# Performance work log

Measured on AMD Instinct MI355X. Metric: run time of the kernel, lower is better.

Reference implementation:

```python
import jax, jax.numpy as jnp
import numpy as np

N_NODES = 30000
N_REL = 8
N_EDGES = 150000
EMB = 128
HID = 128
OUT = 256
HEADS = 4
RANK = 8
SCALE = 1.0
NEG_SLOPE = 0.2
LN_EPS = 1e-5


def setup_inputs():
    key = jax.random.key(0)
    ks = jax.random.split(key, 16)
    def nrm(k, shp, s=0.05):
        return jax.random.normal(k, shp, dtype=jnp.float32) * s
    d2 = HEADS * HID  # conv2 input dim = 512
    return {
        "entity_emb": nrm(ks[0], (N_NODES, EMB)),
        "A1": nrm(ks[1], (N_REL, EMB * RANK)),
        "B1": nrm(ks[2], (N_REL, EMB * RANK)),
        "W1": nrm(ks[3], (HEADS * HID, EMB)),
        "att_l1": nrm(ks[4], (1, HEADS, HID)),
        "att_r1": nrm(ks[5], (1, HEADS, HID)),
        "relb1": jnp.zeros((N_REL, HEADS), jnp.float32),
        "bias1": jnp.zeros((HEADS * HID,), jnp.float32),
        "A2": nrm(ks[6], (N_REL, d2 * RANK)),
        "B2": nrm(ks[7], (N_REL, d2 * RANK)),
        "W2": nrm(ks[8], (OUT, d2)),
        "att_l2": nrm(ks[9], (1, 1, OUT)),
        "att_r2": nrm(ks[10], (1, 1, OUT)),
        "relb2": jnp.zeros((N_REL, 1), jnp.float32),
        "bias2": jnp.zeros((OUT,), jnp.float32),
        "res_W": nrm(ks[11], (OUT, EMB)),
        "res_b": jnp.zeros((OUT,), jnp.float32),
        "ln_g": jnp.ones((OUT,), jnp.float32),
        "ln_b": jnp.zeros((OUT,), jnp.float32),
        "edge_index": jax.random.randint(ks[12], (2, N_EDGES), 0, N_NODES),
        "edge_type": jax.random.randint(ks[13], (N_EDGES,), 0, N_REL),
    }


def _rel_gat_conv(x, A, B, W, att_l, att_r, relb, bias, j_idx, i_idx, etype, heads, out_dim, concat):
    # x: [N,d]; A,B: [R, d*k]; W: [heads*out_dim, d]
    N, d = x.shape
    R = A.shape[0]
    k = RANK
    HC = heads * out_dim
    A3 = A.reshape(R, d, k)
    B3 = B.reshape(R, d, k)
    z_all = x @ W.T  # [N, HC] base linear (shared by z_i and z_j)
    # LoRA low-rank projection per (node, relation): P[n,r] = B_r^T x_n
    P = jnp.einsum('nd,rdk->nrk', x, B3)          # [N,R,k] (small)
    low = P[j_idx, etype]                          # [E,k]
    # Fused LoRA-through-lin: lin(scale*A_r B_r^T x) = scale * low @ (A_r^T W^T)
    M = jnp.einsum('rdk,hd->rkh', A3, W).reshape(R * k, HC)  # [R*k, HC]
    oh = jax.nn.one_hot(etype, R, dtype=x.dtype)   # [E,R]
    low_exp = (oh[:, :, None] * low[:, None, :]).reshape(-1, R * k)  # [E,R*k]
    z_j = (z_all[j_idx] + SCALE * (low_exp @ M)).reshape(-1, heads, out_dim)  # [E,H,C]
    z_i = z_all[i_idx].reshape(-1, heads, out_dim)                            # [E,H,C]
    alpha = (z_i * att_l).sum(-1) + (z_j * att_r).sum(-1) + relb[etype]       # [E,H]
    alpha = jax.nn.leaky_relu(alpha, NEG_SLOPE)
    # per-relation loop => softmax groups are (relation, target node)
    seg = etype * N + i_idx
    n_seg = R * N
    amax = jax.ops.segment_max(alpha, seg, num_segments=n_seg)
    ex = jnp.exp(alpha - amax[seg])
    den = jax.ops.segment_sum(ex, seg, num_segments=n_seg)
    alpha = ex / den[seg]
    msg = z_j * alpha[:, :, None]                  # [E,H,C]
    out = jax.ops.segment_sum(msg, i_idx, num_segments=N)  # [N,H,C]
    out = out.reshape(N, HC) if concat else out.mean(axis=1)
    return out + bias


def _forward(entity_emb, A1, B1, W1, att_l1, att_r1, relb1, bias1,
             A2, B2, W2, att_l2, att_r2, relb2, bias2,
             res_W, res_b, ln_g, ln_b, edge_index, edge_type):
    j_idx, i_idx = edge_index[0], edge_index[1]
    x0 = entity_emb
    x = _rel_gat_conv(x0, A1, B1, W1, att_l1, att_r1, relb1, bias1,
                      j_idx, i_idx, edge_type, HEADS, HID, True)
    x = jax.nn.elu(x)
    x = _rel_gat_conv(x, A2, B2, W2, att_l2, att_r2, relb2, bias2,
                      j_idx, i_idx, edge_type, 1, OUT, False)
    x = x + (x0 @ res_W.T + res_b)
    mu = x.mean(axis=-1, keepdims=True)
    var = ((x - mu) ** 2).mean(axis=-1, keepdims=True)
    return (x - mu) / jnp.sqrt(var + LN_EPS) * ln_g + ln_b


def reference(entity_emb, A1, B1, W1, att_l1, att_r1, relb1, bias1,
              A2, B2, W2, att_l2, att_r2, relb2, bias2,
              res_W, res_b, ln_g, ln_b, edge_index, edge_type):
    return _forward(entity_emb, A1, B1, W1, att_l1, att_r1, relb1, bias1,
                    A2, B2, W2, att_l2, att_r2, relb2, bias2,
                    res_W, res_b, ln_g, ln_b, edge_index, edge_type)
```

## Files before the change

kernel.cpp:

```cpp
#include <hip/hip_runtime.h>
#include <cstddef>

#define NRELS 8
#define EMB 128
#define HID 128
#define OUTD 256
#define HEADS 4
#define RANK 8
#define D2 512
#define KCAT 192
#define NEG_SLOPE 0.2f
#define LN_EPS 1e-5f

typedef short bf16x8 __attribute__((ext_vector_type(8)));
typedef float f32x4 __attribute__((ext_vector_type(4)));

__device__ __forceinline__ unsigned short f2bf(float f) {
  union { float f; unsigned u; } v; v.f = f;
  unsigned u = v.u;
  return (unsigned short)((u + 0x7fffu + ((u >> 16) & 1u)) >> 16);
}
__device__ __forceinline__ float bf2f(unsigned short u) {
  union { unsigned u; float f; } v; v.u = (unsigned)u << 16; return v.f;
}

#define GLOAD16(ldsp, gp) \
  __builtin_amdgcn_global_load_lds((const __attribute__((address_space(1))) unsigned int*)(gp), \
      (__attribute__((address_space(3))) unsigned int*)(ldsp), 16, 0, 0)

template<int ATT, int BIAS, int F32OUT, int PB>
__global__ __launch_bounds__(256) void gemm_tile(const unsigned short* __restrict__ A,
    const unsigned short* __restrict__ B, unsigned short* __restrict__ C,
    float* __restrict__ Cf, const unsigned short* __restrict__ Bp,
    float* __restrict__ Cp, int M, int N, int K, int lda, int aoffc,
    const float* __restrict__ bias, const float* __restrict__ b1p,
    const float* __restrict__ attL, const float* __restrict__ attR,
    float* __restrict__ al, float* __restrict__ ar) {
  __shared__ unsigned short As[2][128 * 32];
  __shared__ unsigned short Bs[2][128 * 32];
  __shared__ float pL[2][128];
  __shared__ float pR[2][128];
  const int tid = threadIdx.x;
  const int wave = tid >> 6;
  const int lane = tid & 63;
  const int wm = wave & 1;
  const int wn = wave >> 1;
  const int r16 = lane & 15;
  const int quad = lane >> 4;
  const int bm = blockIdx.x * 128;
  const int lr = lane >> 2;
  const int lc = ((lane & 3) ^ ((lane >> 3) & 3)) * 8;
  const int rsw = (quad ^ ((r16 >> 1) & 3)) * 8;
  int ar0 = bm + wave * 32 + lr;      if (ar0 >= M) ar0 = M - 1;
  int ar1 = bm + wave * 32 + 16 + lr; if (ar1 >= M) ar1 = M - 1;

  if (PB && blockIdx.y == (int)gridDim.y - 1) {
    const unsigned short* Ag0 = A + (size_t)ar0 * lda + lc;
    const unsigned short* Ag1 = A + (size_t)ar1 * lda + lc;
    const unsigned short* Bg = Bp + (size_t)(wave * 16 + lr) * K + lc;
    f32x4 accp[4][2] = {};
    GLOAD16(As[0] + wave * 1024, Ag0);
    GLOAD16(As[0] + wave * 1024 + 512, Ag1);
    GLOAD16(Bs[0] + wave * 512, Bg);
    __syncthreads();
    int cur = 0;
    for (int k0 = 0; k0 < K; k0 += 32) {
      if (k0 + 32 < K) {
        GLOAD16(As[cur ^ 1] + wave * 1024, Ag0 + k0 + 32);
        GLOAD16(As[cur ^ 1] + wave * 1024 + 512, Ag1 + k0 + 32);
        GLOAD16(Bs[cur ^ 1] + wave * 512, Bg + k0 + 32);
      }
      bf16x8 af[4], bfr[2];
#pragma unroll
      for (int mi = 0; mi < 4; ++mi)
        af[mi] = *(const bf16x8*)(As[cur] + (wm * 64 + mi * 16 + r16) * 32 + rsw);
#pragma unroll
      for (int ni = 0; ni < 2; ++ni)
        bfr[ni] = *(const bf16x8*)(Bs[cur] + (wn * 32 + ni * 16 + r16) * 32 + rsw);
#pragma unroll
      for (int mi = 0; mi < 4; ++mi)
#pragma unroll
        for (int ni = 0; ni < 2; ++ni)
          accp[mi][ni] = __builtin_amdgcn_mfma_f32_16x16x32_bf16(af[mi], bfr[ni], accp[mi][ni], 0, 0, 0);
      __syncthreads();
      cur ^= 1;
    }
#pragma unroll
    for (int mi = 0; mi < 4; ++mi)
#pragma unroll
      for (int ni = 0; ni < 2; ++ni)
#pragma unroll
        for (int r = 0; r < 4; ++r) {
          int row = bm + wm * 64 + mi * 16 + quad * 4 + r;
          if (row < M)
            Cp[(size_t)row * 64 + wn * 32 + ni * 16 + r16] = accp[mi][ni][r];
        }
    return;
  }

  const int bn = blockIdx.y * 128;
  const unsigned short* Abase = A + (size_t)blockIdx.y * aoffc;
  const unsigned short* Ag0 = Abase + (size_t)ar0 * lda + lc;
  const unsigned short* Ag1 = Abase + (size_t)ar1 * lda + lc;
  const unsigned short* Bg0 = B + (size_t)(bn + wave * 32 + lr) * K + lc;
  const unsigned short* Bg1 = B + (size_t)(bn + wave * 32 + 16 + lr) * K + lc;
  f32x4 acc[4][4] = {};
  GLOAD16(As[0] + wave * 1024, Ag0);
  GLOAD16(As[0] + wave * 1024 + 512, Ag1);
  GLOAD16(Bs[0] + wave * 1024, Bg0);
  GLOAD16(Bs[0] + wave * 1024 + 512, Bg1);
  __syncthreads();
  int cur = 0;
  for (int k0 = 0; k0 < K; k0 += 32) {
    if (k0 + 32 < K) {
      GLOAD16(As[cur ^ 1] + wave * 1024, Ag0 + k0 + 32);
      GLOAD16(As[cur ^ 1] + wave * 1024 + 512, Ag1 + k0 + 32);
      GLOAD16(Bs[cur ^ 1] + wave * 1024, Bg0 + k0 + 32);
      GLOAD16(Bs[cur ^ 1] + wave * 1024 + 512, Bg1 + k0 + 32);
    }
    bf16x8 af[4], bfr[4];
#pragma unroll
    for (int mi = 0; mi < 4; ++mi)
      af[mi] = *(const bf16x8*)(As[cur] + (wm * 64 + mi * 16 + r16) * 32 + rsw);
#pragma unroll
    for (int ni = 0; ni < 4; ++ni)
      bfr[ni] = *(const bf16x8*)(Bs[cur] + (wn * 64 + ni * 16 + r16) * 32 + rsw);
#pragma unroll
    for (int mi = 0; mi < 4; ++mi)
#pragma unroll
      for (int ni = 0; ni < 4; ++ni)
        acc[mi][ni] = __builtin_amdgcn_mfma_f32_16x16x32_bf16(af[mi], bfr[ni], acc[mi][ni], 0, 0, 0);
    __syncthreads();
    cur ^= 1;
  }
  float bcol[4];
  if (BIAS) {
#pragma unroll
    for (int ni = 0; ni < 4; ++ni) {
      int cn = bn + wn * 64 + ni * 16 + r16;
      bcol[ni] = bias[cn];
      if (F32OUT) bcol[ni] += b1p[cn];
    }
  }
#pragma unroll
  for (int mi = 0; mi < 4; ++mi)
#pragma unroll
    for (int ni = 0; ni < 4; ++ni)
#pragma unroll
      for (int r = 0; r < 4; ++r) {
        int row = bm + wm * 64 + mi * 16 + quad * 4 + r;
        if (row < M) {
          float v = acc[mi][ni][r];
          if (BIAS) v += bcol[ni];
          size_t idx = (size_t)row * N + bn + wn * 64 + ni * 16 + r16;
          if (F32OUT) Cf[idx] = v;
          else        C[idx] = f2bf(v);
        }
      }
  if (ATT) {
    float La[4], Ra[4];
#pragma unroll
    for (int ni = 0; ni < 4; ++ni) {
      int cn = bn + wn * 64 + ni * 16 + r16;
      La[ni] = attL[cn]; Ra[ni] = attR[cn];
    }
#pragma unroll
    for (int mi = 0; mi < 4; ++mi)
#pragma unroll
      for (int r = 0; r < 4; ++r) {
        float sl = 0.f, sr = 0.f;
#pragma unroll
        for (int ni = 0; ni < 4; ++ni) {
          sl = fmaf(acc[mi][ni][r], La[ni], sl);
          sr = fmaf(acc[mi][ni][r], Ra[ni], sr);
        }
#pragma unroll
        for (int o = 1; o < 16; o <<= 1) {
          sl += __shfl_xor(sl, o, 64);
          sr += __shfl_xor(sr, o, 64);
        }
        if (r16 == 0) {
          int rl = wm * 64 + mi * 16 + quad * 4 + r;
          pL[wn][rl] = sl; pR[wn][rl] = sr;
        }
      }
    __syncthreads();
    if (tid < 128) {
      int row = bm + tid;
      if (row < M) {
        float sl = pL[0][tid] + pL[1][tid];
        float sr = pR[0][tid] + pR[1][tid];
        if (ATT == 1) {
          al[(size_t)row * 4 + blockIdx.y] = sl;
          ar[(size_t)row * 4 + blockIdx.y] = sr;
        } else {
          al[(size_t)blockIdx.y * M + row] = sl;
          ar[(size_t)blockIdx.y * M + row] = sr;
        }
      }
    }
  }
}

__global__ __launch_bounds__(256) void gemm_abt2(const float* __restrict__ Amat1,
    const float* __restrict__ W1, float* __restrict__ M1o,
    const float* __restrict__ Amat2, const float* __restrict__ W2, float* __restrict__ M2o) {
  const float* A; const float* B; float* C; int N, K, bn;
  if (blockIdx.x < D2 / 64) { A = Amat1; B = W1; C = M1o; N = D2; K = EMB; bn = blockIdx.x * 64; }
  else { A = Amat2; B = W2; C = M2o; N = OUTD; K = D2; bn = (blockIdx.x - D2 / 64) * 64; }
  __shared__ float As[32][64];
  __shared__ float Bs[32][64];
  const int tid = threadIdx.x;
  const int tx = tid & 15;
  const int ty = tid >> 4;
  const int lr = tid & 63;
  const int lq = tid >> 6;
  float acc[4][4] = {};
  for (int k0 = 0; k0 < K; k0 += 32) {
#pragma unroll
    for (int s = 0; s < 2; ++s) {
      const int q = lq + s * 4;
      float4 va = *(const float4*)(A + (size_t)lr * K + k0 + q * 4);
      As[q * 4 + 0][lr] = va.x; As[q * 4 + 1][lr] = va.y;
      As[q * 4 + 2][lr] = va.z; As[q * 4 + 3][lr] = va.w;
      float4 vb = *(const float4*)(B + (size_t)(bn + lr) * K + k0 + q * 4);
      Bs[q * 4 + 0][lr] = vb.x; Bs[q * 4 + 1][lr] = vb.y;
      Bs[q * 4 + 2][lr] = vb.z; Bs[q * 4 + 3][lr] = vb.w;
    }
    __syncthreads();
#pragma unroll
    for (int kk = 0; kk < 32; ++kk) {
      float a[4], b[4];
#pragma unroll
      for (int i2 = 0; i2 < 4; ++i2) { a[i2] = As[kk][ty * 4 + i2]; b[i2] = Bs[kk][tx * 4 + i2]; }
#pragma unroll
      for (int i2 = 0; i2 < 4; ++i2)
#pragma unroll
        for (int j2 = 0; j2 < 4; ++j2)
          acc[i2][j2] = fmaf(a[i2], b[j2], acc[i2][j2]);
    }
    __syncthreads();
  }
#pragma unroll
  for (int i2 = 0; i2 < 4; ++i2)
#pragma unroll
    for (int j2 = 0; j2 < 4; ++j2)
      C[(size_t)(ty * 4 + i2) * N + bn + tx * 4 + j2] = acc[i2][j2];
}

__global__ void prep_all(const float* __restrict__ x0, const float* __restrict__ W1,
    const float* __restrict__ W2, const float* __restrict__ res_W,
    const float* __restrict__ A1, const float* __restrict__ A2,
    const float* __restrict__ B1, const float* __restrict__ B2,
    unsigned short* __restrict__ x0b, unsigned short* __restrict__ Acat,
    unsigned short* __restrict__ W1b, unsigned short* __restrict__ W2b,
    unsigned short* __restrict__ RWcat,
    float* __restrict__ Amat1, float* __restrict__ Amat2,
    unsigned short* __restrict__ Bmat1b, unsigned short* __restrict__ Bmat2b,
    const int* __restrict__ ii, int* __restrict__ ideg, int* __restrict__ prepos,
    int E, int nx0) {
  int idx = blockIdx.x * 256 + threadIdx.x;
  if (idx < E) { prepos[idx] = atomicAdd(&ideg[ii[idx]], 1); return; } idx -= E;
  if (idx < nx0) { unsigned short b = f2bf(x0[idx]); x0b[idx] = b;
    Acat[(size_t)(idx >> 7) * KCAT + (idx & 127)] = b; return; } idx -= nx0;
  if (idx < D2 * EMB) { W1b[idx] = f2bf(W1[idx]); return; } idx -= D2 * EMB;
  if (idx < OUTD * D2) { W2b[idx] = f2bf(W2[idx]); return; } idx -= OUTD * D2;
  if (idx < OUTD * EMB) { RWcat[(size_t)(idx >> 7) * KCAT + (idx & 127)] = f2bf(res_W[idx]); return; } idx -= OUTD * EMB;
  if (idx < 64 * EMB) { int d = idx % EMB, rk = idx / EMB, k = rk & 7, r = rk >> 3;
    Amat1[idx] = A1[(size_t)r * EMB * RANK + (size_t)d * RANK + k]; return; } idx -= 64 * EMB;
  if (idx < 64 * D2) { int d = idx % D2, rk = idx / D2, k = rk & 7, r = rk >> 3;
    Amat2[idx] = A2[(size_t)r * D2 * RANK + (size_t)d * RANK + k]; return; } idx -= 64 * D2;
  if (idx < 64 * EMB) { int d = idx % EMB, rk = idx / EMB, k = rk & 7, r = rk >> 3;
    Bmat1b[idx] = f2bf(B1[(size_t)r * EMB * RANK + (size_t)d * RANK + k]); return; } idx -= 64 * EMB;
  if (idx < 64 * D2) { int d = idx % D2, rk = idx / D2, k = rk & 7, r = rk >> 3;
    Bmat2b[idx] = f2bf(B2[(size_t)r * D2 * RANK + (size_t)d * RANK + k]); }
}

__global__ void fold_build(const float* __restrict__ M1, const float* __restrict__ M2,
                           const float* __restrict__ attR1, const float* __restrict__ attR2,
                           unsigned short* __restrict__ M1T2, unsigned short* __restrict__ RWcat,
                           float* __restrict__ Matt1, float* __restrict__ Matt2) {
  int idx = blockIdx.x * 256 + threadIdx.x;
  if (idx < 512 * 64) { int c = idx >> 6, rk = idx & 63;
    M1T2[idx] = f2bf(M1[(size_t)rk * D2 + c]); return; } idx -= 512 * 64;
  if (idx < 256 * 64) { int c = idx >> 6, rk = idx & 63;
    RWcat[(size_t)c * KCAT + 128 + rk] = f2bf(M2[(size_t)rk * OUTD + c]); return; } idx -= 256 * 64;
  if (idx < 256) { int h = idx & 3, rk = idx >> 2;
    float s = 0.f;
    for (int c = 0; c < HID; ++c)
      s = fmaf(M1[(size_t)rk * D2 + h * HID + c], attR1[h * HID + c], s);
    Matt1[rk * 4 + h] = s; return; } idx -= 256;
  if (idx < 64) {
    float s = 0.f;
    for (int c = 0; c < OUTD; ++c) s = fmaf(M2[(size_t)idx * OUTD + c], attR2[c], s);
    Matt2[idx] = s; }
}

__global__ __launch_bounds__(1024) void exscan_kernel(const int* __restrict__ deg,
                                                      int* __restrict__ rowstart, int n) {
  __shared__ int wsum[16];
  int t = threadIdx.x;
  int lane = t & 63, wid = t >> 6;
  int carry = 0;
  for (int base = 0; base < n; base += 4096) {
    int i0 = base + t * 4;
    int v0 = 0, v1 = 0, v2 = 0, v3 = 0;
    if (i0 + 3 < n) {
      int4 vv = *(const int4*)(deg + i0);
      v0 = vv.x; v1 = vv.y; v2 = vv.z; v3 = vv.w;
    } else {
      if (i0 < n) v0 = deg[i0];
      if (i0 + 1 < n) v1 = deg[i0 + 1];
      if (i0 + 2 < n) v2 = deg[i0 + 2];
      if (i0 + 3 < n) v3 = deg[i0 + 3];
    }
    int tot = v0 + v1 + v2 + v3;
    int x = tot;
#pragma unroll
    for (int o = 1; o < 64; o <<= 1) {
      int y = __shfl_up(x, o, 64);
      if (lane >= o) x += y;
    }
    if (lane == 63) wsum[wid] = x;
    __syncthreads();
    if (t == 0) {
      int s = carry;
      for (int w2 = 0; w2 < 16; ++w2) { int tmp = wsum[w2]; wsum[w2] = s; s += tmp; }
      carry = s;
    }
    __syncthreads();
    int ex0 = x - tot + wsum[wid];
    if (i0 + 3 < n) {
      int4 ov; ov.x = ex0; ov.y = ex0 + v0; ov.z = ex0 + v0 + v1; ov.w = ex0 + v0 + v1 + v2;
      *(int4*)(rowstart + i0) = ov;
    } else {
      if (i0 < n) rowstart[i0] = ex0;
      if (i0 + 1 < n) rowstart[i0 + 1] = ex0 + v0;
      if (i0 + 2 < n) rowstart[i0 + 2] = ex0 + v0 + v1;
      if (i0 + 3 < n) rowstart[i0 + 3] = ex0 + v0 + v1 + v2;
    }
    __syncthreads();
  }
  if (t == 0) rowstart[n] = carry;
}

__global__ void edge_alpha1(const int* __restrict__ ji, const int* __restrict__ ii,
                            const int* __restrict__ et, const int* __restrict__ rowstart,
                            const int* __restrict__ prepos,
                            const float* __restrict__ P1,
                            const float* __restrict__ al1, const float* __restrict__ ar1,
                            const float* __restrict__ relb1, const float* __restrict__ Matt1,
                            float4* __restrict__ recs1, int E) {
  int e = blockIdx.x * blockDim.x + threadIdx.x;
  if (e >= E) return;
  int j = ji[e], i = ii[e], rt = et[e];
  float4 lo0 = *(const float4*)(P1 + (size_t)j * 64 + rt * 8);
  float4 lo1 = *(const float4*)(P1 + (size_t)j * 64 + rt * 8 + 4);
  float low[RANK] = {lo0.x, lo0.y, lo0.z, lo0.w, lo1.x, lo1.y, lo1.z, lo1.w};
  float4 ali = *(const float4*)(al1 + (size_t)i * 4);
  float4 arj = *(const float4*)(ar1 + (size_t)j * 4);
  float4 rb  = *(const float4*)(relb1 + rt * 4);
  float a0 = ali.x + arj.x + rb.x;
  float a1 = ali.y + arj.y + rb.y;
  float a2 = ali.z + arj.z + rb.z;
  float a3 = ali.w + arj.w + rb.w;
#pragma unroll
  for (int k = 0; k < RANK; ++k) {
    float4 mk = *(const float4*)(Matt1 + ((rt * 8 + k) << 2));
    a0 = fmaf(low[k], mk.x, a0); a1 = fmaf(low[k], mk.y, a1);
    a2 = fmaf(low[k], mk.z, a2); a3 = fmaf(low[k], mk.w, a3);
  }
  a0 = (a0 > 0.f) ? a0 : NEG_SLOPE * a0;
  a1 = (a1 > 0.f) ? a1 : NEG_SLOPE * a1;
  a2 = (a2 > 0.f) ? a2 : NEG_SLOPE * a2;
  a3 = (a3 > 0.f) ? a3 : NEG_SLOPE * a3;
  float e0 = expf(a0), e1 = expf(a1), e2 = expf(a2), e3 = expf(a3);
  float4* rp = recs1 + (size_t)(rowstart[i] + prepos[e]) * 4;
  rp[0] = make_float4(__int_as_float(j), e0, e1, e2);
  rp[1] = make_float4(e3, __int_as_float(rt), low[0], low[1]);
  rp[2] = make_float4(low[2], low[3], low[4], low[5]);
  rp[3] = make_float4(low[6], low[7], 0.f, 0.f);
}

__global__ __launch_bounds__(256) void qden1(const float4* __restrict__ recs1,
    const int* __restrict__ rowstart, unsigned short* __restrict__ Q1b,
    float* __restrict__ rden1, int Nn) {
  const int wid = threadIdx.x >> 6, lane = threadIdx.x & 63;
  const int i = blockIdx.x * 4 + wid;
  if (i >= Nn) return;
  const int rt_mine = lane >> 3, k = lane & 7;
  const int s0 = rowstart[i], deg = rowstart[i + 1] - s0;
  const float* rf = (const float*)recs1;
  float q0 = 0.f, q1 = 0.f, q2 = 0.f, q3 = 0.f;
  float d0 = 0.f, d1 = 0.f, d2 = 0.f, d3 = 0.f;
  float4 a0 = {}, a1 = {};
  float lw = 0.f;
  if (deg > 0) {
    a0 = recs1[(size_t)s0 * 4]; a1 = recs1[(size_t)s0 * 4 + 1];
    lw = rf[(size_t)s0 * 16 + 6 + k];
  }
  for (int p = 0; p < deg; ++p) {
    float4 b0 = a0, b1 = a1; float lwn = lw;
    if (p + 1 < deg) {
      b0 = recs1[(size_t)(s0 + p + 1) * 4]; b1 = recs1[(size_t)(s0 + p + 1) * 4 + 1];
      lwn = rf[(size_t)(s0 + p + 1) * 16 + 6 + k];
    }
    int rt = __float_as_int(a1.y);
    if (rt == rt_mine) {
      q0 = fmaf(a0.y, lw, q0); q1 = fmaf(a0.z, lw, q1);
      q2 = fmaf(a0.w, lw, q2); q3 = fmaf(a1.x, lw, q3);
      d0 += a0.y; d1 += a0.z; d2 += a0.w; d3 += a1.x;
    }
    a0 = b0; a1 = b1; lw = lwn;
  }
  float r0 = (d0 > 0.f) ? 1.f / d0 : 0.f;
  float r1 = (d1 > 0.f) ? 1.f / d1 : 0.f;
  float r2 = (d2 > 0.f) ? 1.f / d2 : 0.f;
  float r3 = (d3 > 0.f) ? 1.f / d3 : 0.f;
  size_t qb = (size_t)i * 256;
  Q1b[qb + lane]       = f2bf(q0 * r0);
  Q1b[qb + 64 + lane]  = f2bf(q1 * r1);
  Q1b[qb + 128 + lane] = f2bf(q2 * r2);
  Q1b[qb + 192 + lane] = f2bf(q3 * r3);
  if (k == 0) {
    size_t db = (size_t)i * 32;
    rden1[db + rt_mine]      = r0;
    rden1[db + 8 + rt_mine]  = r1;
    rden1[db + 16 + rt_mine] = r2;
    rden1[db + 24 + rt_mine] = r3;
  }
}

__global__ __launch_bounds__(256) void node_agg1_lite(const float4* __restrict__ recs1,
    const int* __restrict__ rowstart, const unsigned short* __restrict__ z1b,
    const unsigned short* __restrict__ L1b, const float* __restrict__ rden1,
    unsigned short* __restrict__ h1out, int Nn) {
  const int wid = threadIdx.x >> 6;
  const int lane = threadIdx.x & 63;
  const int i = blockIdx.x * 4 + wid;
  if (i >= Nn) return;
  __shared__ float denS[4][32];
  if (lane < 32) denS[wid][lane] = rden1[(size_t)i * 32 + lane];
  const int s0 = rowstart[i];
  const int deg = rowstart[i + 1] - s0;
  const int c0 = lane * 8;
  const float* rf = (const float*)recs1;
  const int hb = (lane >> 4) << 3;
  float acc[8] = {};
  float4 r0 = {}, r1 = {}, r2 = {};
  float2 g0 = {}, g1 = {}, g2 = {};
  uint4 za = {}, zb = {};
  if (deg > 0) { r0 = recs1[(size_t)s0 * 4]; g0 = *(const float2*)(rf + (size_t)s0 * 16 + 4);
    za = *(const uint4*)(z1b + (size_t)__float_as_int(r0.x) * D2 + c0); }
  if (deg > 1) { r1 = recs1[(size_t)(s0 + 1) * 4]; g1 = *(const float2*)(rf + (size_t)(s0 + 1) * 16 + 4);
    zb = *(const uint4*)(z1b + (size_t)__float_as_int(r1.x) * D2 + c0); }
  if (deg > 2) { r2 = recs1[(size_t)(s0 + 2) * 4]; g2 = *(const float2*)(rf + (size_t)(s0 + 2) * 16 + 4); }
  for (int p = 0; p < deg; ++p) {
    float4 r3 = r2; float2 g3 = g2; uint4 zn = zb;
    if (p + 3 < deg) { r3 = recs1[(size_t)(s0 + p + 3) * 4];
                       g3 = *(const float2*)(rf + (size_t)(s0 + p + 3) * 16 + 4); }
    if (p + 2 < deg) zn = *(const uint4*)(z1b + (size_t)__float_as_int(r2.x) * D2 + c0);
    int rt = __float_as_int(g0.y);
    float wlo = (lane & 16) ? r0.z : r0.y;
    float whi = (lane & 16) ? g0.x : r0.w;
    float wt = ((lane & 32) ? whi : wlo) * denS[wid][hb + rt];
    acc[0] = fmaf(wt, bf2f((unsigned short)(za.x & 0xffff)), acc[0]);
    acc[1] = fmaf(wt, bf2f((unsigned short)(za.x >> 16)), acc[1]);
    acc[2] = fmaf(wt, bf2f((unsigned short)(za.y & 0xffff)), acc[2]);
    acc[3] = fmaf(wt, bf2f((unsigned short)(za.y >> 16)), acc[3]);
    acc[4] = fmaf(wt, bf2f((unsigned short)(za.z & 0xffff)), acc[4]);
    acc[5] = fmaf(wt, bf2f((unsigned short)(za.z >> 16)), acc[5]);
    acc[6] = fmaf(wt, bf2f((unsigned short)(za.w & 0xffff)), acc[6]);
    acc[7] = fmaf(wt, bf2f((unsigned short)(za.w >> 16)), acc[7]);
    r0 = r1; g0 = g1; r1 = r2; g1 = g2; r2 = r3; g2 = g3; za = zb; zb = zn;
  }
  uint4 lv = *(const uint4*)(L1b + (size_t)i * D2 + c0);
  unsigned lw[4] = {lv.x, lv.y, lv.z, lv.w};
  unsigned ov[4];
#pragma unroll
  for (int q = 0; q < 4; ++q) {
    float e0 = acc[2 * q]     + bf2f((unsigned short)(lw[q] & 0xffff));
    float e1 = acc[2 * q + 1] + bf2f((unsigned short)(lw[q] >> 16));
    e0 = e0 > 0.f ? e0 : expm1f(e0);
    e1 = e1 > 0.f ? e1 : expm1f(e1);
    ov[q] = (unsigned)f2bf(e0) | ((unsigned)f2bf(e1) << 16);
  }
  *(uint4*)(h1out + (size_t)i * D2 + c0) = make_uint4(ov[0], ov[1], ov[2], ov[3]);
}

__global__ void edge_alpha2(const int* __restrict__ ji, const int* __restrict__ ii,
                            const int* __restrict__ et, const int* __restrict__ rowstart,
                            const int* __restrict__ prepos,
                            const float* __restrict__ P2,
                            const float* __restrict__ al2, const float* __restrict__ ar2,
                            const float* __restrict__ relb2, const float* __restrict__ Matt2,
                            float4* __restrict__ recs2, int E, int Nn) {
  int e = blockIdx.x * blockDim.x + threadIdx.x;
  if (e >= E) return;
  int j = ji[e], i = ii[e], rt = et[e];
  float4 lo0 = *(const float4*)(P2 + (size_t)j * 64 + rt * 8);
  float4 lo1 = *(const float4*)(P2 + (size_t)j * 64 + rt * 8 + 4);
  float low[RANK] = {lo0.x, lo0.y, lo0.z, lo0.w, lo1.x, lo1.y, lo1.z, lo1.w};
  float a = al2[i] + al2[(size_t)Nn + i] + ar2[j] + ar2[(size_t)Nn + j] + relb2[rt];
#pragma unroll
  for (int k = 0; k < RANK; ++k) a = fmaf(low[k], Matt2[rt * RANK + k], a);
  a = (a > 0.f) ? a : NEG_SLOPE * a;
  float ex = expf(a);
  float4* rp = recs2 + (size_t)(rowstart[i] + prepos[e]) * 3;
  rp[0] = make_float4(__int_as_float(j), __int_as_float(rt), ex, low[0]);
  rp[1] = make_float4(low[1], low[2], low[3], low[4]);
  rp[2] = make_float4(low[5], low[6], low[7], 0.f);
}

__global__ __launch_bounds__(256) void qden2(const float4* __restrict__ recs2,
    const int* __restrict__ rowstart, unsigned short* __restrict__ Acat,
    float* __restrict__ rden2, int Nn) {
  const int wid = threadIdx.x >> 6, lane = threadIdx.x & 63;
  const int i = blockIdx.x * 4 + wid;
  if (i >= Nn) return;
  const int rt_mine = lane >> 3, k = lane & 7;
  const int s0 = rowstart[i], deg = rowstart[i + 1] - s0;
  const float* rf = (const float*)recs2;
  float q = 0.f, d = 0.f;
  float4 a0 = {}; float lw = 0.f;
  if (deg > 0) { a0 = recs2[(size_t)s0 * 3]; lw = rf[(size_t)s0 * 12 + 3 + k]; }
  for (int p = 0; p < deg; ++p) {
    float4 b0 = a0; float lwn = lw;
    if (p + 1 < deg) {
      b0 = recs2[(size_t)(s0 + p + 1) * 3];
      lwn = rf[(size_t)(s0 + p + 1) * 12 + 3 + k];
    }
    int rt = __float_as_int(a0.y);
    if (rt == rt_mine) { q = fmaf(a0.z, lw, q); d += a0.z; }
    a0 = b0; lw = lwn;
  }
  float rd = (d > 0.f) ? 1.f / d : 0.f;
  Acat[(size_t)i * KCAT + 128 + lane] = f2bf(q * rd);
  if (k == 0) rden2[(size_t)i * 8 + rt_mine] = rd;
}

__global__ __launch_bounds__(256) void node_agg2_lite(const float4* __restrict__ recs2,
    const int* __restrict__ rowstart, const unsigned short* __restrict__ z2b,
    const float* __restrict__ rden2, const float* __restrict__ o2,
    const float* __restrict__ ln_g, const float* __restrict__ ln_b,
    float* __restrict__ y, int Nn) {
  const int wid = threadIdx.x >> 6;
  const int lane = threadIdx.x & 63;
  const int i = blockIdx.x * 4 + wid;
  if (i >= Nn) return;
  __shared__ float denS[4][NRELS];
  if (lane < NRELS) denS[wid][lane] = rden2[(size_t)i * 8 + lane];
  const int s0 = rowstart[i];
  const int deg = rowstart[i + 1] - s0;
  const int c0 = lane * 4;
  float acc[4] = {};
  float4 r0 = {}, r1 = {}, r2 = {};
  uint2 za = make_uint2(0u, 0u), zb = make_uint2(0u, 0u);
  if (deg > 0) { r0 = recs2[(size_t)s0 * 3];
    za = *(const uint2*)(z2b + (size_t)__float_as_int(r0.x) * OUTD + c0); }
  if (deg > 1) { r1 = recs2[(size_t)(s0 + 1) * 3];
    zb = *(const uint2*)(z2b + (size_t)__float_as_int(r1.x) * OUTD + c0); }
  if (deg > 2) r2 = recs2[(size_t)(s0 + 2) * 3];
  for (int p = 0; p < deg; ++p) {
    float4 r3 = r2;
    uint2 zn = zb;
    if (p + 3 < deg) r3 = recs2[(size_t)(s0 + p + 3) * 3];
    if (p + 2 < deg)
      zn = *(const uint2*)(z2b + (size_t)__float_as_int(r2.x) * OUTD + c0);
    int rt = __float_as_int(r0.y);
    float wt = r0.z * denS[wid][rt];
    acc[0] = fmaf(wt, bf2f((unsigned short)(za.x & 0xffff)), acc[0]);
    acc[1] = fmaf(wt, bf2f((unsigned short)(za.x >> 16)), acc[1]);
    acc[2] = fmaf(wt, bf2f((unsigned short)(za.y & 0xffff)), acc[2]);
    acc[3] = fmaf(wt, bf2f((unsigned short)(za.y >> 16)), acc[3]);
    r0 = r1; r1 = r2; r2 = r3; za = zb; zb = zn;
  }
  float4 rsv = *(const float4*)(o2 + (size_t)i * OUTD + c0);
  float vv[4];
  vv[0] = acc[0] + rsv.x;
  vv[1] = acc[1] + rsv.y;
  vv[2] = acc[2] + rsv.z;
  vv[3] = acc[3] + rsv.w;
  float s = vv[0] + vv[1] + vv[2] + vv[3];
  for (int o = 32; o > 0; o >>= 1) s += __shfl_xor(s, o, 64);
  float mu = s * (1.f / OUTD);
  float q = 0.f;
#pragma unroll
  for (int k = 0; k < 4; ++k) { float d = vv[k] - mu; q += d * d; }
  for (int o = 32; o > 0; o >>= 1) q += __shfl_xor(q, o, 64);
  float rstd = rsqrtf(q * (1.f / OUTD) + LN_EPS);
  float4 g = *(const float4*)(ln_g + c0);
  float4 bb = *(const float4*)(ln_b + c0);
  float4 ov;
  ov.x = (vv[0] - mu) * rstd * g.x + bb.x;
  ov.y = (vv[1] - mu) * rstd * g.y + bb.y;
  ov.z = (vv[2] - mu) * rstd * g.z + bb.z;
  ov.w = (vv[3] - mu) * rstd * g.w + bb.w;
  *(float4*)(y + (size_t)i * OUTD + c0) = ov;
}

extern "C" void kernel_launch(void* const* d_in, const int* in_sizes, int n_in,
                              void* d_out, int out_size, void* d_ws, size_t ws_size,
                              hipStream_t stream) {
  const float* x0     = (const float*)d_in[0];
  const float* A1     = (const float*)d_in[1];
  const float* B1     = (const float*)d_in[2];
  const float* W1     = (const float*)d_in[3];
  const float* attL1  = (const float*)d_in[4];
  const float* attR1  = (const float*)d_in[5];
  const float* relb1  = (const float*)d_in[6];
  const float* bias1  = (const float*)d_in[7];
  const float* A2     = (const float*)d_in[8];
  const float* B2     = (const float*)d_in[9];
  const float* W2     = (const float*)d_in[10];
  const float* attL2  = (const float*)d_in[11];
  const float* attR2  = (const float*)d_in[12];
  const float* relb2  = (const float*)d_in[13];
  const float* bias2  = (const float*)d_in[14];
  const float* res_W  = (const float*)d_in[15];
  const float* res_b  = (const float*)d_in[16];
  const float* ln_g   = (const float*)d_in[17];
  const float* ln_b   = (const float*)d_in[18];
  const int*   eidx   = (const int*)d_in[19];
  const int*   etype  = (const int*)d_in[20];
  float* out = (float*)d_out;

  const int Nn = in_sizes[0] / EMB;
  const int E  = in_sizes[20];
  const int* ji = eidx;
  const int* ii = eidx + E;

  float* w = (float*)d_ws;
  size_t off = 0;
  float* o2    = w + off; off += (size_t)Nn * OUTD;
  float* P1    = w + off; off += (size_t)Nn * 64;
  float* P2    = w + off; off += (size_t)Nn * 64;
  float* M1    = w + off; off += 64 * D2;
  float* M2    = w + off; off += 64 * OUTD;
  float* Amat1 = w + off; off += 64 * EMB;
  float* Amat2 = w + off; off += 64 * D2;
  float* Matt1 = w + off; off += 64 * 4;
  float* Matt2 = w + off; off += 64;
  float* al1   = w + off; off += (size_t)Nn * 4;
  float* ar1   = w + off; off += (size_t)Nn * 4;
  float* al2   = w + off; off += (size_t)Nn * 2;
  float* ar2   = w + off; off += (size_t)Nn * 2;
  float* rden1 = w + off; off += (size_t)Nn * 32;
  float* rden2 = w + off; off += (size_t)Nn * 8;
  float4* recs1 = (float4*)(w + off); off += (size_t)E * 16;
  float4* recs2 = (float4*)(w + off); off += (size_t)E * 12;
  unsigned short* z1b    = (unsigned short*)(w + off); off += (size_t)Nn * D2 / 2;
  unsigned short* z2b    = (unsigned short*)(w + off); off += (size_t)Nn * OUTD / 2;
  unsigned short* x0b    = (unsigned short*)(w + off); off += (size_t)Nn * EMB / 2;
  unsigned short* h1b    = (unsigned short*)(w + off); off += (size_t)Nn * D2 / 2;
  unsigned short* W1b    = (unsigned short*)(w + off); off += (size_t)D2 * EMB / 2;
  unsigned short* W2b    = (unsigned short*)(w + off); off += (size_t)OUTD * D2 / 2;
  unsigned short* Bmat1b = (unsigned short*)(w + off); off += (size_t)64 * EMB / 2;
  unsigned short* Bmat2b = (unsigned short*)(w + off); off += (size_t)64 * D2 / 2;
  unsigned short* Acat   = (unsigned short*)(w + off); off += (size_t)Nn * KCAT / 2;
  unsigned short* RWcat  = (unsigned short*)(w + off); off += (size_t)OUTD * KCAT / 2;
  unsigned short* M1T2   = (unsigned short*)(w + off); off += (size_t)512 * 64 / 2;
  int* ideg     = (int*)(w + off); off += (size_t)Nn;
  int* prepos   = (int*)(w + off); off += (size_t)E;
  int* rowstart = (int*)(w + off); off += (size_t)Nn + 1;
  (void)ws_size; (void)n_in; (void)out_size;

  unsigned short* Q1b = (unsigned short*)P1;
  unsigned short* L1b = (unsigned short*)o2;

  const int MT128 = (Nn + 127) / 128;
  const int NB4 = (Nn + 3) / 4;

  (void)hipMemsetAsync(ideg, 0, (size_t)Nn * sizeof(int), stream);
  {
    int nx0 = Nn * EMB;
    int total = E + nx0 + D2 * EMB + OUTD * D2 + OUTD * EMB
              + 64 * EMB + 64 * D2 + 64 * EMB + 64 * D2;
    prep_all<<<(total + 255) / 256, 256, 0, stream>>>(x0, W1, W2, res_W, A1, A2, B1, B2,
        x0b, Acat, W1b, W2b, RWcat, Amat1, Amat2, Bmat1b, Bmat2b, ii, ideg, prepos, E, nx0);
  }
  exscan_kernel<<<1, 1024, 0, stream>>>(ideg, rowstart, Nn);

  gemm_abt2<<<dim3(D2 / 64 + OUTD / 64, 1), 256, 0, stream>>>(Amat1, W1, M1, Amat2, W2, M2);
  fold_build<<<(512 * 64 + 256 * 64 + 256 + 64 + 255) / 256, 256, 0, stream>>>(
      M1, M2, attR1, attR2, M1T2, RWcat, Matt1, Matt2);

  gemm_tile<1, 0, 0, 1><<<dim3(MT128, D2 / 128 + 1), 256, 0, stream>>>(x0b, W1b, z1b, nullptr,
      Bmat1b, P1, Nn, D2, EMB, EMB, 0, nullptr, nullptr, attL1, attR1, al1, ar1);

  edge_alpha1<<<(E + 255) / 256, 256, 0, stream>>>(ji, ii, etype, rowstart, prepos, P1,
                                                   al1, ar1, relb1, Matt1, recs1, E);
  qden1<<<NB4, 256, 0, stream>>>(recs1, rowstart, Q1b, rden1, Nn);
  gemm_tile<0, 1, 0, 0><<<dim3(MT128, D2 / 128), 256, 0, stream>>>(Q1b, M1T2, L1b, nullptr,
      nullptr, nullptr, Nn, D2, 64, 256, 64, bias1, nullptr, nullptr, nullptr, nullptr, nullptr);
  node_agg1_lite<<<NB4, 256, 0, stream>>>(recs1, rowstart, z1b, L1b, rden1, h1b, Nn);

  gemm_tile<2, 0, 0, 1><<<dim3(MT128, OUTD / 128 + 1), 256, 0, stream>>>(h1b, W2b, z2b, nullptr,
      Bmat2b, P2, Nn, OUTD, D2, D2, 0, nullptr, nullptr, attL2, attR2, al2, ar2);

  edge_alpha2<<<(E + 255) / 256, 256, 0, stream>>>(ji, ii, etype, rowstart, prepos, P2,
                                                   al2, ar2, relb2, Matt2, recs2, E, Nn);
  qden2<<<NB4, 256, 0, stream>>>(recs2, rowstart, Acat, rden2, Nn);
  gemm_tile<0, 1, 1, 0><<<dim3(MT128, OUTD / 128), 256, 0, stream>>>(Acat, RWcat, nullptr, o2,
      nullptr, nullptr, Nn, OUTD, KCAT, KCAT, 0, bias2, res_b, nullptr, nullptr, nullptr, nullptr);
  node_agg2_lite<<<NB4, 256, 0, stream>>>(recs2, rowstart, z2b, rden2, o2, ln_g, ln_b, out, Nn);
}
```

Measured before the change: 367.5 us.

## Aggregate raw x0 in layer 1 and fold attention vectors into projection GEMMs

Layer 1 no longer materialises z1 = x0·W1ᵀ before aggregation. Each node now gathers the 128-wide bf16 x0 rows per head together with the normalized LoRA low-rank sums into a concatenated [N,4×192] buffer. A single GEMM against [W1 | M1ᵀ] then applies bias and ELU in its epilogue. The attention logits are folded into precomputed W·att rows appended to the LoRA B matrix, so the small projection GEMM emits P, al and ar together, and the separate attention-reduction epilogue is removed. This trades a 512-wide gather and an extra z1 GEMM plus a Q/L GEMM for a narrower gather and one larger-K GEMM, at the cost of a 768-wide intermediate and padded zero rows in the projection matrices.

```diff
diff --git a/kernel.cpp b/kernel.cpp
--- a/kernel.cpp
+++ b/kernel.cpp
@@ -28,18 +28,14 @@
   __builtin_amdgcn_global_load_lds((const __attribute__((address_space(1))) unsigned int*)(gp), \
       (__attribute__((address_space(3))) unsigned int*)(ldsp), 16, 0, 0)
 
-template<int ATT, int BIAS, int F32OUT, int PB>
+template<int BIAS, int F32OUT, int ELU, int PB>
 __global__ __launch_bounds__(256) void gemm_tile(const unsigned short* __restrict__ A,
     const unsigned short* __restrict__ B, unsigned short* __restrict__ C,
     float* __restrict__ Cf, const unsigned short* __restrict__ Bp,
     float* __restrict__ Cp, int M, int N, int K, int lda, int aoffc,
-    const float* __restrict__ bias, const float* __restrict__ b1p,
-    const float* __restrict__ attL, const float* __restrict__ attR,
-    float* __restrict__ al, float* __restrict__ ar) {
+    const float* __restrict__ bias, const float* __restrict__ b1p) {
   __shared__ unsigned short As[2][128 * 32];
   __shared__ unsigned short Bs[2][128 * 32];
-  __shared__ float pL[2][128];
-  __shared__ float pR[2][128];
   const int tid = threadIdx.x;
   const int wave = tid >> 6;
   const int lane = tid & 63;
@@ -51,59 +47,16 @@
   const int lr = lane >> 2;
   const int lc = ((lane & 3) ^ ((lane >> 3) & 3)) * 8;
   const int rsw = (quad ^ ((r16 >> 1) & 3)) * 8;
+  const bool isP = PB && (blockIdx.y == (int)gridDim.y - 1);
+  const unsigned short* Bu = isP ? Bp : B;
+  const int bn = isP ? 0 : blockIdx.y * 128;
+  const unsigned short* Abase = A + (size_t)blockIdx.y * (isP ? 0 : aoffc);
   int ar0 = bm + wave * 32 + lr;      if (ar0 >= M) ar0 = M - 1;
   int ar1 = bm + wave * 32 + 16 + lr; if (ar1 >= M) ar1 = M - 1;
-
-  if (PB && blockIdx.y == (int)gridDim.y - 1) {
-    const unsigned short* Ag0 = A + (size_t)ar0 * lda + lc;
-    const unsigned short* Ag1 = A + (size_t)ar1 * lda + lc;
-    const unsigned short* Bg = Bp + (size_t)(wave * 16 + lr) * K + lc;
-    f32x4 accp[4][2] = {};
-    GLOAD16(As[0] + wave * 1024, Ag0);
-    GLOAD16(As[0] + wave * 1024 + 512, Ag1);
-    GLOAD16(Bs[0] + wave * 512, Bg);
-    __syncthreads();
-    int cur = 0;
-    for (int k0 = 0; k0 < K; k0 += 32) {
-      if (k0 + 32 < K) {
-        GLOAD16(As[cur ^ 1] + wave * 1024, Ag0 + k0 + 32);
-        GLOAD16(As[cur ^ 1] + wave * 1024 + 512, Ag1 + k0 + 32);
-        GLOAD16(Bs[cur ^ 1] + wave * 512, Bg + k0 + 32);
-      }
-      bf16x8 af[4], bfr[2];
-#pragma unroll
-      for (int mi = 0; mi < 4; ++mi)
-        af[mi] = *(const bf16x8*)(As[cur] + (wm * 64 + mi * 16 + r16) * 32 + rsw);
-#pragma unroll
-      for (int ni = 0; ni < 2; ++ni)
-        bfr[ni] = *(const bf16x8*)(Bs[cur] + (wn * 32 + ni * 16 + r16) * 32 + rsw);
-#pragma unroll
-      for (int mi = 0; mi < 4; ++mi)
-#pragma unroll
-        for (int ni = 0; ni < 2; ++ni)
-          accp[mi][ni] = __builtin_amdgcn_mfma_f32_16x16x32_bf16(af[mi], bfr[ni], accp[mi][ni], 0, 0, 0);
-      __syncthreads();
-      cur ^= 1;
-    }
-#pragma unroll
-    for (int mi = 0; mi < 4; ++mi)
-#pragma unroll
-      for (int ni = 0; ni < 2; ++ni)
-#pragma unroll
-        for (int r = 0; r < 4; ++r) {
-          int row = bm + wm * 64 + mi * 16 + quad * 4 + r;
-          if (row < M)
-            Cp[(size_t)row * 64 + wn * 32 + ni * 16 + r16] = accp[mi][ni][r];
-        }
-    return;
-  }
-
-  const int bn = blockIdx.y * 128;
-  const unsigned short* Abase = A + (size_t)blockIdx.y * aoffc;
   const unsigned short* Ag0 = Abase + (size_t)ar0 * lda + lc;
   const unsigned short* Ag1 = Abase + (size_t)ar1 * lda + lc;
-  const unsigned short* Bg0 = B + (size_t)(bn + wave * 32 + lr) * K + lc;
-  const unsigned short* Bg1 = B + (size_t)(bn + wave * 32 + 16 + lr) * K + lc;
+  const unsigned short* Bg0 = Bu + (size_t)(bn + wave * 32 + lr) * K + lc;
+  const unsigned short* Bg1 = Bu + (size_t)(bn + wave * 32 + 16 + lr) * K + lc;
   f32x4 acc[4][4] = {};
   GLOAD16(As[0] + wave * 1024, Ag0);
   GLOAD16(As[0] + wave * 1024 + 512, Ag1);
@@ -150,56 +103,19 @@
       for (int r = 0; r < 4; ++r) {
         int row = bm + wm * 64 + mi * 16 + quad * 4 + r;
         if (row < M) {
+          int col = wn * 64 + ni * 16 + r16;
           float v = acc[mi][ni][r];
-          if (BIAS) v += bcol[ni];
-          size_t idx = (size_t)row * N + bn + wn * 64 + ni * 16 + r16;
-          if (F32OUT) Cf[idx] = v;
-          else        C[idx] = f2bf(v);
+          if (isP) {
+            Cp[(size_t)row * 128 + col] = v;
+          } else {
+            if (BIAS) v += bcol[ni];
+            if (ELU) v = v > 0.f ? v : expm1f(v);
+            size_t idx = (size_t)row * N + bn + col;
+            if (F32OUT) Cf[idx] = v;
+            else        C[idx] = f2bf(v);
+          }
         }
       }
-  if (ATT) {
-    float La[4], Ra[4];
-#pragma unroll
-    for (int ni = 0; ni < 4; ++ni) {
-      int cn = bn + wn * 64 + ni * 16 + r16;
-      La[ni] = attL[cn]; Ra[ni] = attR[cn];
-    }
-#pragma unroll
-    for (int mi = 0; mi < 4; ++mi)
-#pragma unroll
-      for (int r = 0; r < 4; ++r) {
-        float sl = 0.f, sr = 0.f;
-#pragma unroll
-        for (int ni = 0; ni < 4; ++ni) {
-          sl = fmaf(acc[mi][ni][r], La[ni], sl);
-          sr = fmaf(acc[mi][ni][r], Ra[ni], sr);
-        }
-#pragma unroll
-        for (int o = 1; o < 16; o <<= 1) {
-          sl += __shfl_xor(sl, o, 64);
-          sr += __shfl_xor(sr, o, 64);
-        }
-        if (r16 == 0) {
-          int rl = wm * 64 + mi * 16 + quad * 4 + r;
-          pL[wn][rl] = sl; pR[wn][rl] = sr;
-        }
-      }
-    __syncthreads();
-    if (tid < 128) {
-      int row = bm + tid;
-      if (row < M) {
-        float sl = pL[0][tid] + pL[1][tid];
-        float sr = pR[0][tid] + pR[1][tid];
-        if (ATT == 1) {
-          al[(size_t)row * 4 + blockIdx.y] = sl;
-          ar[(size_t)row * 4 + blockIdx.y] = sr;
-        } else {
-          al[(size_t)blockIdx.y * M + row] = sl;
-          ar[(size_t)blockIdx.y * M + row] = sr;
-        }
-      }
-    }
-  }
 }
 
 __global__ __launch_bounds__(256) void gemm_abt2(const float* __restrict__ Amat1,
@@ -248,13 +164,12 @@
       C[(size_t)(ty * 4 + i2) * N + bn + tx * 4 + j2] = acc[i2][j2];
 }
 
-__global__ void prep_all(const float* __restrict__ x0, const float* __restrict__ W1,
-    const float* __restrict__ W2, const float* __restrict__ res_W,
+__global__ void prep_all(const float* __restrict__ x0, const float* __restrict__ W2,
+    const float* __restrict__ res_W,
     const float* __restrict__ A1, const float* __restrict__ A2,
     const float* __restrict__ B1, const float* __restrict__ B2,
     unsigned short* __restrict__ x0b, unsigned short* __restrict__ Acat,
-    unsigned short* __restrict__ W1b, unsigned short* __restrict__ W2b,
-    unsigned short* __restrict__ RWcat,
+    unsigned short* __restrict__ W2b, unsigned short* __restrict__ RWcat,
     float* __restrict__ Amat1, float* __restrict__ Amat2,
     unsigned short* __restrict__ Bmat1b, unsigned short* __restrict__ Bmat2b,
     const int* __restrict__ ii, int* __restrict__ ideg, int* __restrict__ prepos,
@@ -263,7 +178,6 @@
   if (idx < E) { prepos[idx] = atomicAdd(&ideg[ii[idx]], 1); return; } idx -= E;
   if (idx < nx0) { unsigned short b = f2bf(x0[idx]); x0b[idx] = b;
     Acat[(size_t)(idx >> 7) * KCAT + (idx & 127)] = b; return; } idx -= nx0;
-  if (idx < D2 * EMB) { W1b[idx] = f2bf(W1[idx]); return; } idx -= D2 * EMB;
   if (idx < OUTD * D2) { W2b[idx] = f2bf(W2[idx]); return; } idx -= OUTD * D2;
   if (idx < OUTD * EMB) { RWcat[(size_t)(idx >> 7) * KCAT + (idx & 127)] = f2bf(res_W[idx]); return; } idx -= OUTD * EMB;
   if (idx < 64 * EMB) { int d = idx % EMB, rk = idx / EMB, k = rk & 7, r = rk >> 3;
@@ -277,14 +191,40 @@
 }
 
 __global__ void fold_build(const float* __restrict__ M1, const float* __restrict__ M2,
-                           const float* __restrict__ attR1, const float* __restrict__ attR2,
-                           unsigned short* __restrict__ M1T2, unsigned short* __restrict__ RWcat,
-                           float* __restrict__ Matt1, float* __restrict__ Matt2) {
+    const float* __restrict__ W1, const float* __restrict__ W2,
+    const float* __restrict__ attL1, const float* __restrict__ attR1,
+    const float* __restrict__ attL2, const float* __restrict__ attR2,
+    const unsigned short* __restrict__ Bmat1b, const unsigned short* __restrict__ Bmat2b,
+    unsigned short* __restrict__ Bcat1, unsigned short* __restrict__ RWcat,
+    unsigned short* __restrict__ Bp1ext, unsigned short* __restrict__ Bp2ext,
+    float* __restrict__ Matt1, float* __restrict__ Matt2) {
   int idx = blockIdx.x * 256 + threadIdx.x;
-  if (idx < 512 * 64) { int c = idx >> 6, rk = idx & 63;
-    M1T2[idx] = f2bf(M1[(size_t)rk * D2 + c]); return; } idx -= 512 * 64;
+  if (idx < 512 * 192) { int c = idx / 192, t = idx % 192;
+    float v = (t < 128) ? W1[(size_t)c * EMB + t] : M1[(size_t)(t - 128) * D2 + c];
+    Bcat1[idx] = f2bf(v); return; } idx -= 512 * 192;
   if (idx < 256 * 64) { int c = idx >> 6, rk = idx & 63;
     RWcat[(size_t)c * KCAT + 128 + rk] = f2bf(M2[(size_t)rk * OUTD + c]); return; } idx -= 256 * 64;
+  if (idx < 128 * 128) { int r = idx >> 7, d = idx & 127;
+    unsigned short v;
+    if (r < 64) v = Bmat1b[r * 128 + d];
+    else if (r < 72) { int h = (r - 64) & 3;
+      const float* att = (r < 68) ? attL1 : attR1;
+      float s = 0.f;
+      for (int c = 0; c < HID; ++c)
+        s = fmaf(W1[(size_t)(h * HID + c) * EMB + d], att[h * HID + c], s);
+      v = f2bf(s); }
+    else v = 0;
+    Bp1ext[idx] = v; return; } idx -= 128 * 128;
+  if (idx < 128 * 512) { int r = idx >> 9, d = idx & 511;
+    unsigned short v;
+    if (r < 64) v = Bmat2b[r * 512 + d];
+    else if (r < 66) { const float* att = (r == 64) ? attL2 : attR2;
+      float s = 0.f;
+      for (int c = 0; c < OUTD; ++c)
+        s = fmaf(W2[(size_t)c * D2 + d], att[c], s);
+      v = f2bf(s); }
+    else v = 0;
+    Bp2ext[idx] = v; return; } idx -= 128 * 512;
   if (idx < 256) { int h = idx & 3, rk = idx >> 2;
     float s = 0.f;
     for (int c = 0; c < HID; ++c)
@@ -347,18 +287,17 @@
 __global__ void edge_alpha1(const int* __restrict__ ji, const int* __restrict__ ii,
                             const int* __restrict__ et, const int* __restrict__ rowstart,
                             const int* __restrict__ prepos,
-                            const float* __restrict__ P1,
-                            const float* __restrict__ al1, const float* __restrict__ ar1,
+                            const float* __restrict__ Cp1,
                             const float* __restrict__ relb1, const float* __restrict__ Matt1,
                             float4* __restrict__ recs1, int E) {
   int e = blockIdx.x * blockDim.x + threadIdx.x;
   if (e >= E) return;
   int j = ji[e], i = ii[e], rt = et[e];
-  float4 lo0 = *(const float4*)(P1 + (size_t)j * 64 + rt * 8);
-  float4 lo1 = *(const float4*)(P1 + (size_t)j * 64 + rt * 8 + 4);
+  float4 lo0 = *(const float4*)(Cp1 + (size_t)j * 128 + rt * 8);
+  float4 lo1 = *(const float4*)(Cp1 + (size_t)j * 128 + rt * 8 + 4);
   float low[RANK] = {lo0.x, lo0.y, lo0.z, lo0.w, lo1.x, lo1.y, lo1.z, lo1.w};
-  float4 ali = *(const float4*)(al1 + (size_t)i * 4);
-  float4 arj = *(const float4*)(ar1 + (size_t)j * 4);
+  float4 ali = *(const float4*)(Cp1 + (size_t)i * 128 + 64);
+  float4 arj = *(const float4*)(Cp1 + (size_t)j * 128 + 68);
   float4 rb  = *(const float4*)(relb1 + rt * 4);
   float a0 = ali.x + arj.x + rb.x;
   float a1 = ali.y + arj.y + rb.y;
@@ -382,126 +321,101 @@
   rp[3] = make_float4(low[6], low[7], 0.f, 0.f);
 }
 
-__global__ __launch_bounds__(256) void qden1(const float4* __restrict__ recs1,
-    const int* __restrict__ rowstart, unsigned short* __restrict__ Q1b,
-    float* __restrict__ rden1, int Nn) {
+__global__ __launch_bounds__(256) void agg1f(const float4* __restrict__ recs1,
+    const int* __restrict__ rowstart, const unsigned short* __restrict__ x0b,
+    unsigned short* __restrict__ XQ1, int Nn) {
+  __shared__ float denS[4][32];
   const int wid = threadIdx.x >> 6, lane = threadIdx.x & 63;
   const int i = blockIdx.x * 4 + wid;
   if (i >= Nn) return;
   const int rt_mine = lane >> 3, k = lane & 7;
   const int s0 = rowstart[i], deg = rowstart[i + 1] - s0;
   const float* rf = (const float*)recs1;
-  float q0 = 0.f, q1 = 0.f, q2 = 0.f, q3 = 0.f;
-  float d0 = 0.f, d1 = 0.f, d2 = 0.f, d3 = 0.f;
-  float4 a0 = {}, a1 = {};
-  float lw = 0.f;
-  if (deg > 0) {
-    a0 = recs1[(size_t)s0 * 4]; a1 = recs1[(size_t)s0 * 4 + 1];
-    lw = rf[(size_t)s0 * 16 + 6 + k];
-  }
+  const size_t xb = (size_t)i * 768;
+  {
+    float q0 = 0.f, q1 = 0.f, q2 = 0.f, q3 = 0.f;
+    float d0 = 0.f, d1 = 0.f, d2 = 0.f, d3 = 0.f;
+    float4 a0 = {}, a1 = {};
+    float lw = 0.f;
+    if (deg > 0) {
+      a0 = recs1[(size_t)s0 * 4]; a1 = recs1[(size_t)s0 * 4 + 1];
+      lw = rf[(size_t)s0 * 16 + 6 + k];
+    }
+    for (int p = 0; p < deg; ++p) {
+      float4 b0 = a0, b1 = a1; float lwn = lw;
+      if (p + 1 < deg) {
+        b0 = recs1[(size_t)(s0 + p + 1) * 4]; b1 = recs1[(size_t)(s0 + p + 1) * 4 + 1];
+        lwn = rf[(size_t)(s0 + p + 1) * 16 + 6 + k];
+      }
+      int rt = __float_as_int(a1.y);
+      if (rt == rt_mine) {
+        q0 = fmaf(a0.y, lw, q0); q1 = fmaf(a0.z, lw, q1);
+        q2 = fmaf(a0.w, lw, q2); q3 = fmaf(a1.x, lw, q3);
+        d0 += a0.y; d1 += a0.z; d2 += a0.w; d3 += a1.x;
+      }
+      a0 = b0; a1 = b1; lw = lwn;
+    }
+    float r0 = (d0 > 0.f) ? 1.f / d0 : 0.f;
+    float r1 = (d1 > 0.f) ? 1.f / d1 : 0.f;
+    float r2 = (d2 > 0.f) ? 1.f / d2 : 0.f;
+    float r3 = (d3 > 0.f) ? 1.f / d3 : 0.f;
+    XQ1[xb + 0 * 192 + 128 + lane] = f2bf(q0 * r0);
+    XQ1[xb + 1 * 192 + 128 + lane] = f2bf(q1 * r1);
+    XQ1[xb + 2 * 192 + 128 + lane] = f2bf(q2 * r2);
+    XQ1[xb + 3 * 192 + 128 + lane] = f2bf(q3 * r3);
+    if (k == 0) {
+      denS[wid][rt_mine]      = r0;
+      denS[wid][8 + rt_mine]  = r1;
+      denS[wid][16 + rt_mine] = r2;
+      denS[wid][24 + rt_mine] = r3;
+    }
+  }
+  const int c0 = lane * 2;
+  float acc[8] = {};
+  float4 r0 = {}, r1 = {};
+  float2 g0 = {}, g1 = {};
+  unsigned za = 0u, zn0 = 0u;
+  if (deg > 0) { r0 = recs1[(size_t)s0 * 4]; g0 = *(const float2*)(rf + (size_t)s0 * 16 + 4);
+    za = *(const unsigned*)(x0b + (size_t)__float_as_int(r0.x) * 128 + c0); }
+  if (deg > 1) { r1 = recs1[(size_t)(s0 + 1) * 4]; g1 = *(const float2*)(rf + (size_t)(s0 + 1) * 16 + 4); }
   for (int p = 0; p < deg; ++p) {
-    float4 b0 = a0, b1 = a1; float lwn = lw;
-    if (p + 1 < deg) {
-      b0 = recs1[(size_t)(s0 + p + 1) * 4]; b1 = recs1[(size_t)(s0 + p + 1) * 4 + 1];
-      lwn = rf[(size_t)(s0 + p + 1) * 16 + 6 + k];
-    }
-    int rt = __float_as_int(a1.y);
-    if (rt == rt_mine) {
-      q0 = fmaf(a0.y, lw, q0); q1 = fmaf(a0.z, lw, q1);
-      q2 = fmaf(a0.w, lw, q2); q3 = fmaf(a1.x, lw, q3);
-      d0 += a0.y; d1 += a0.z; d2 += a0.w; d3 += a1.x;
-    }
-    a0 = b0; a1 = b1; lw = lwn;
-  }
-  float r0 = (d0 > 0.f) ? 1.f / d0 : 0.f;
-  float r1 = (d1 > 0.f) ? 1.f / d1 : 0.f;
-  float r2 = (d2 > 0.f) ? 1.f / d2 : 0.f;
-  float r3 = (d3 > 0.f) ? 1.f / d3 : 0.f;
-  size_t qb = (size_t)i * 256;
-  Q1b[qb + lane]       = f2bf(q0 * r0);
-  Q1b[qb + 64 + lane]  = f2bf(q1 * r1);
-  Q1b[qb + 128 + lane] = f2bf(q2 * r2);
-  Q1b[qb + 192 + lane] = f2bf(q3 * r3);
-  if (k == 0) {
-    size_t db = (size_t)i * 32;
-    rden1[db + rt_mine]      = r0;
-    rden1[db + 8 + rt_mine]  = r1;
-    rden1[db + 16 + rt_mine] = r2;
-    rden1[db + 24 + rt_mine] = r3;
-  }
-}
-
-__global__ __launch_bounds__(256) void node_agg1_lite(const float4* __restrict__ recs1,
-    const int* __restrict__ rowstart, const unsigned short* __restrict__ z1b,
-    const unsigned short* __restrict__ L1b, const float* __restrict__ rden1,
-    unsigned short* __restrict__ h1out, int Nn) {
-  const int wid = threadIdx.x >> 6;
-  const int lane = threadIdx.x & 63;
-  const int i = blockIdx.x * 4 + wid;
-  if (i >= Nn) return;
-  __shared__ float denS[4][32];
-  if (lane < 32) denS[wid][lane] = rden1[(size_t)i * 32 + lane];
-  const int s0 = rowstart[i];
-  const int deg = rowstart[i + 1] - s0;
-  const int c0 = lane * 8;
-  const float* rf = (const float*)recs1;
-  const int hb = (lane >> 4) << 3;
-  float acc[8] = {};
-  float4 r0 = {}, r1 = {}, r2 = {};
-  float2 g0 = {}, g1 = {}, g2 = {};
-  uint4 za = {}, zb = {};
-  if (deg > 0) { r0 = recs1[(size_t)s0 * 4]; g0 = *(const float2*)(rf + (size_t)s0 * 16 + 4);
-    za = *(const uint4*)(z1b + (size_t)__float_as_int(r0.x) * D2 + c0); }
-  if (deg > 1) { r1 = recs1[(size_t)(s0 + 1) * 4]; g1 = *(const float2*)(rf + (size_t)(s0 + 1) * 16 + 4);
-    zb = *(const uint4*)(z1b + (size_t)__float_as_int(r1.x) * D2 + c0); }
-  if (deg > 2) { r2 = recs1[(size_t)(s0 + 2) * 4]; g2 = *(const float2*)(rf + (size_t)(s0 + 2) * 16 + 4); }
-  for (int p = 0; p < deg; ++p) {
-    float4 r3 = r2; float2 g3 = g2; uint4 zn = zb;
-    if (p + 3 < deg) { r3 = recs1[(size_t)(s0 + p + 3) * 4];
-                       g3 = *(const float2*)(rf + (size_t)(s0 + p + 3) * 16 + 4); }
-    if (p + 2 < deg) zn = *(const uint4*)(z1b + (size_t)__float_as_int(r2.x) * D2 + c0);
+    float4 r2 = r1; float2 g2 = g1; unsigned zb = za;
+    if (p + 2 < deg) { r2 = recs1[(size_t)(s0 + p + 2) * 4];
+                       g2 = *(const float2*)(rf + (size_t)(s0 + p + 2) * 16 + 4); }
+    if (p + 1 < deg) zb = *(const unsigned*)(x0b + (size_t)__float_as_int(r1.x) * 128 + c0);
     int rt = __float_as_int(g0.y);
-    float wlo = (lane & 16) ? r0.z : r0.y;
-    float whi = (lane & 16) ? g0.x : r0.w;
-    float wt = ((lane & 32) ? whi : wlo) * denS[wid][hb + rt];
-    acc[0] = fmaf(wt, bf2f((unsigned short)(za.x & 0xffff)), acc[0]);
-    acc[1] = fmaf(wt, bf2f((unsigned short)(za.x >> 16)), acc[1]);
-    acc[2] = fmaf(wt, bf2f((unsigned short)(za.y & 0xffff)), acc[2]);
-    acc[3] = fmaf(wt, bf2f((unsigned short)(za.y >> 16)), acc[3]);
-    acc[4] = fmaf(wt, bf2f((unsigned short)(za.z & 0xffff)), acc[4]);
-    acc[5] = fmaf(wt, bf2f((unsigned short)(za.z >> 16)), acc[5]);
-    acc[6] = fmaf(wt, bf2f((unsigned short)(za.w & 0xffff)), acc[6]);
-    acc[7] = fmaf(wt, bf2f((unsigned short)(za.w >> 16)), acc[7]);
-    r0 = r1; g0 = g1; r1 = r2; g1 = g2; r2 = r3; g2 = g3; za = zb; zb = zn;
-  }
-  uint4 lv = *(const uint4*)(L1b + (size_t)i * D2 + c0);
-  unsigned lw[4] = {lv.x, lv.y, lv.z, lv.w};
-  unsigned ov[4];
-#pragma unroll
-  for (int q = 0; q < 4; ++q) {
-    float e0 = acc[2 * q]     + bf2f((unsigned short)(lw[q] & 0xffff));
-    float e1 = acc[2 * q + 1] + bf2f((unsigned short)(lw[q] >> 16));
-    e0 = e0 > 0.f ? e0 : expm1f(e0);
-    e1 = e1 > 0.f ? e1 : expm1f(e1);
-    ov[q] = (unsigned)f2bf(e0) | ((unsigned)f2bf(e1) << 16);
-  }
-  *(uint4*)(h1out + (size_t)i * D2 + c0) = make_uint4(ov[0], ov[1], ov[2], ov[3]);
+    float w0 = r0.y * denS[wid][rt];
+    float w1 = r0.z * denS[wid][8 + rt];
+    float w2 = r0.w * denS[wid][16 + rt];
+    float w3 = g0.x * denS[wid][24 + rt];
+    float v0 = bf2f((unsigned short)(za & 0xffff));
+    float v1 = bf2f((unsigned short)(za >> 16));
+    acc[0] = fmaf(w0, v0, acc[0]); acc[1] = fmaf(w0, v1, acc[1]);
+    acc[2] = fmaf(w1, v0, acc[2]); acc[3] = fmaf(w1, v1, acc[3]);
+    acc[4] = fmaf(w2, v0, acc[4]); acc[5] = fmaf(w2, v1, acc[5]);
+    acc[6] = fmaf(w3, v0, acc[6]); acc[7] = fmaf(w3, v1, acc[7]);
+    r0 = r1; g0 = g1; r1 = r2; g1 = g2; za = zb;
+  }
+#pragma unroll
+  for (int h = 0; h < 4; ++h) {
+    unsigned pv = (unsigned)f2bf(acc[2 * h]) | ((unsigned)f2bf(acc[2 * h + 1]) << 16);
+    *(unsigned*)(XQ1 + xb + h * 192 + c0) = pv;
+  }
 }
 
 __global__ void edge_alpha2(const int* __restrict__ ji, const int* __restrict__ ii,
                             const int* __restrict__ et, const int* __restrict__ rowstart,
                             const int* __restrict__ prepos,
-                            const float* __restrict__ P2,
-                            const float* __restrict__ al2, const float* __restrict__ ar2,
+                            const float* __restrict__ Cp2,
                             const float* __restrict__ relb2, const float* __restrict__ Matt2,
-                            float4* __restrict__ recs2, int E, int Nn) {
+                            float4* __restrict__ recs2, int E) {
   int e = blockIdx.x * blockDim.x + threadIdx.x;
   if (e >= E) return;
   int j = ji[e], i = ii[e], rt = et[e];
-  float4 lo0 = *(const float4*)(P2 + (size_t)j * 64 + rt * 8);
-  float4 lo1 = *(const float4*)(P2 + (size_t)j * 64 + rt * 8 + 4);
+  float4 lo0 = *(const float4*)(Cp2 + (size_t)j * 128 + rt * 8);
+  float4 lo1 = *(const float4*)(Cp2 + (size_t)j * 128 + rt * 8 + 4);
   float low[RANK] = {lo0.x, lo0.y, lo0.z, lo0.w, lo1.x, lo1.y, lo1.z, lo1.w};
-  float a = al2[i] + al2[(size_t)Nn + i] + ar2[j] + ar2[(size_t)Nn + j] + relb2[rt];
+  float a = Cp2[(size_t)i * 128 + 64] + Cp2[(size_t)j * 128 + 65] + relb2[rt];
 #pragma unroll
   for (int k = 0; k < RANK; ++k) a = fmaf(low[k], Matt2[rt * RANK + k], a);
   a = (a > 0.f) ? a : NEG_SLOPE * a;
@@ -633,75 +547,69 @@
   float* w = (float*)d_ws;
   size_t off = 0;
   float* o2    = w + off; off += (size_t)Nn * OUTD;
-  float* P1    = w + off; off += (size_t)Nn * 64;
-  float* P2    = w + off; off += (size_t)Nn * 64;
+  float* Cp1   = w + off; off += (size_t)Nn * 128;
+  float* Cp2   = w + off; off += (size_t)Nn * 128;
   float* M1    = w + off; off += 64 * D2;
   float* M2    = w + off; off += 64 * OUTD;
   float* Amat1 = w + off; off += 64 * EMB;
   float* Amat2 = w + off; off += 64 * D2;
   float* Matt1 = w + off; off += 64 * 4;
   float* Matt2 = w + off; off += 64;
-  float* al1   = w + off; off += (size_t)Nn * 4;
-  float* ar1   = w + off; off += (size_t)Nn * 4;
-  float* al2   = w + off; off += (size_t)Nn * 2;
-  float* ar2   = w + off; off += (size_t)Nn * 2;
-  float* rden1 = w + off; off += (size_t)Nn * 32;
   float* rden2 = w + off; off += (size_t)Nn * 8;
   float4* recs1 = (float4*)(w + off); off += (size_t)E * 16;
   float4* recs2 = (float4*)(w + off); off += (size_t)E * 12;
-  unsigned short* z1b    = (unsigned short*)(w + off); off += (size_t)Nn * D2 / 2;
   unsigned short* z2b    = (unsigned short*)(w + off); off += (size_t)Nn * OUTD / 2;
   unsigned short* x0b    = (unsigned short*)(w + off); off += (size_t)Nn * EMB / 2;
   unsigned short* h1b    = (unsigned short*)(w + off); off += (size_t)Nn * D2 / 2;
-  unsigned short* W1b    = (unsigned short*)(w + off); off += (size_t)D2 * EMB / 2;
+  unsigned short* XQ1    = (unsigned short*)(w + off); off += (size_t)Nn * 768 / 2;
   unsigned short* W2b    = (unsigned short*)(w + off); off += (size_t)OUTD * D2 / 2;
   unsigned short* Bmat1b = (unsigned short*)(w + off); off += (size_t)64 * EMB / 2;
   unsigned short* Bmat2b = (unsigned short*)(w + off); off += (size_t)64 * D2 / 2;
   unsigned short* Acat   = (unsigned short*)(w + off); off += (size_t)Nn * KCAT / 2;
   unsigned short* RWcat  = (unsigned short*)(w + off); off += (size_t)OUTD * KCAT / 2;
-  unsigned short* M1T2   = (unsigned short*)(w + off); off += (size_t)512 * 64 / 2;
+  unsigned short* Bcat1  = (unsigned short*)(w + off); off += (size_t)512 * 192 / 2;
+  unsigned short* Bp1ext = (unsigned short*)(w + off); off += (size_t)128 * 128 / 2;
+  unsigned short* Bp2ext = (unsigned short*)(w + off); off += (size_t)128 * 512 / 2;
   int* ideg     = (int*)(w + off); off += (size_t)Nn;
   int* prepos   = (int*)(w + off); off += (size_t)E;
   int* rowstart = (int*)(w + off); off += (size_t)Nn + 1;
   (void)ws_size; (void)n_in; (void)out_size;
 
-  unsigned short* Q1b = (unsigned short*)P1;
-  unsigned short* L1b = (unsigned short*)o2;
-
   const int MT128 = (Nn + 127) / 128;
   const int NB4 = (Nn + 3) / 4;
 
   (void)hipMemsetAsync(ideg, 0, (size_t)Nn * sizeof(int), stream);
   {
     int nx0 = Nn * EMB;
-    int total = E + nx0 + D2 * EMB + OUTD * D2 + OUTD * EMB
-              + 64 * EMB + 64 * D2 + 64 * EMB + 64 * D2;
-    prep_all<<<(total + 255) / 256, 256, 0, stream>>>(x0, W1, W2, res_W, A1, A2, B1, B2,
-        x0b, Acat, W1b, W2b, RWcat, Amat1, Amat2, Bmat1b, Bmat2b, ii, ideg, prepos, E, nx0);
+    int total = E + nx0 + OUTD * D2 + OUTD * EMB + 64 * EMB + 64 * D2 + 64 * EMB + 64 * D2;
+    prep_all<<<(total + 255) / 256, 256, 0, stream>>>(x0, W2, res_W, A1, A2, B1, B2,
+        x0b, Acat, W2b, RWcat, Amat1, Amat2, Bmat1b, Bmat2b, ii, ideg, prepos, E, nx0);
   }
   exscan_kernel<<<1, 1024, 0, stream>>>(ideg, rowstart, Nn);
 
   gemm_abt2<<<dim3(D2 / 64 + OUTD / 64, 1), 256, 0, stream>>>(Amat1, W1, M1, Amat2, W2, M2);
-  fold_build<<<(512 * 64 + 256 * 64 + 256 + 64 + 255) / 256, 256, 0, stream>>>(
-      M1, M2, attR1, attR2, M1T2, RWcat, Matt1, Matt2);
-
-  gemm_tile<1, 0, 0, 1><<<dim3(MT128, D2 / 128 + 1), 256, 0, stream>>>(x0b, W1b, z1b, nullptr,
-      Bmat1b, P1, Nn, D2, EMB, EMB, 0, nullptr, nullptr, attL1, attR1, al1, ar1);
-
-  edge_alpha1<<<(E + 255) / 256, 256, 0, stream>>>(ji, ii, etype, rowstart, prepos, P1,
-                                                   al1, ar1, relb1, Matt1, recs1, E);
-  qden1<<<NB4, 256, 0, stream>>>(recs1, rowstart, Q1b, rden1, Nn);
-  gemm_tile<0, 1, 0, 0><<<dim3(MT128, D2 / 128), 256, 0, stream>>>(Q1b, M1T2, L1b, nullptr,
-      nullptr, nullptr, Nn, D2, 64, 256, 64, bias1, nullptr, nullptr, nullptr, nullptr, nullptr);
-  node_agg1_lite<<<NB4, 256, 0, stream>>>(recs1, rowstart, z1b, L1b, rden1, h1b, Nn);
-
-  gemm_tile<2, 0, 0, 1><<<dim3(MT128, OUTD / 128 + 1), 256, 0, stream>>>(h1b, W2b, z2b, nullptr,
-      Bmat2b, P2, Nn, OUTD, D2, D2, 0, nullptr, nullptr, attL2, attR2, al2, ar2);
-
-  edge_alpha2<<<(E + 255) / 256, 256, 0, stream>>>(ji, ii, etype, rowstart, prepos, P2,
-                                                   al2, ar2, relb2, Matt2, recs2, E, Nn);
+  {
+    int total = 512 * 192 + 256 * 64 + 128 * 128 + 128 * 512 + 256 + 64;
+    fold_build<<<(total + 255) / 256, 256, 0, stream>>>(M1, M2, W1, W2, attL1, attR1,
+        attL2, attR2, Bmat1b, Bmat2b, Bcat1, RWcat, Bp1ext, Bp2ext, Matt1, Matt2);
+  }
+
+  gemm_tile<0, 1, 0, 0><<<dim3(MT128, 1), 256, 0, stream>>>(x0b, Bp1ext, nullptr, Cp1,
+      nullptr, nullptr, Nn, 128, EMB, EMB, 0, nullptr, nullptr);
+
+  edge_alpha1<<<(E + 255) / 256, 256, 0, stream>>>(ji, ii, etype, rowstart, prepos, Cp1,
+                                                   relb1, Matt1, recs1, E);
+  agg1f<<<NB4, 256, 0, stream>>>(recs1, rowstart, x0b, XQ1, Nn);
+  gemm_tile<1, 0, 1, 0><<<dim3(MT128, 4), 256, 0, stream>>>(XQ1, Bcat1, h1b, nullptr,
+      nullptr, nullptr, Nn, D2, 192, 768, 192, bias1, nullptr);
+
+  gemm_tile<0, 0, 0, 1><<<dim3(MT128, 3), 256, 0, stream>>>(h1b, W2b, z2b, nullptr,
+      Bp2ext, Cp2, Nn, OUTD, D2, D2, 0, nullptr, nullptr);
+
+  edge_alpha2<<<(E + 255) / 256, 256, 0, stream>>>(ji, ii, etype, rowstart, prepos, Cp2,
+                                                   relb2, Matt2, recs2, E);
   qden2<<<NB4, 256, 0, stream>>>(recs2, rowstart, Acat, rden2, Nn);
-  gemm_tile<0, 1, 1, 0><<<dim3(MT128, OUTD / 128), 256, 0, stream>>>(Acat, RWcat, nullptr, o2,
-      nullptr, nullptr, Nn, OUTD, KCAT, KCAT, 0, bias2, res_b, nullptr, nullptr, nullptr, nullptr);
+  gemm_tile<1, 1, 0, 0><<<dim3(MT128, 2), 256, 0, stream>>>(Acat, RWcat, nullptr, o2,
+      nullptr, nullptr, Nn, OUTD, KCAT, KCAT, 0, bias2, res_b);
   node_agg2_lite<<<NB4, 256, 0, stream>>>(recs2, rowstart, z2b, rden2, o2, ln_g, ln_b, out, Nn);
 }
```

Result: faster. 341.5 us (-7.1%).
